# Kernel tuning notes

Hardware: AMD Instinct MI355X
Metric: run time of the kernel (lower is better)

The kernel has to match this reference:

```python
import jax, jax.numpy as jnp
import numpy as np

N = 65536      # total nodes (ground + sub)
NG = 32768     # ground nodes (subnodes are NG..N)
H = 64         # n_hidden
FIN = 32       # n_node_features
L = 2          # num_convolution_blocks
B = 64         # graphs in batch
MAXDEG = 10    # MFConv max_degree -> 11 buckets
EG = 1048576   # ground-graph edges
ES = 1048576   # subgraph edges
EX = 524288    # cross (ground<->sub) edges


def setup_inputs() -> dict:
    key = jax.random.key(0)
    ks = jax.random.split(key, 32)
    NS = N - NG
    x = jax.random.normal(ks[0], (N, FIN), jnp.float32)
    # ground graph: src/dst in [0, NG)
    edge_index = jax.random.randint(ks[1], (2, EG), 0, NG).astype(jnp.int64)
    # subgraph: src/dst in [NG, N)
    subgraph_edge_index = (NG + jax.random.randint(ks[2], (2, ES), 0, NS)).astype(jnp.int64)
    # ground -> sub
    ns_src = jax.random.randint(ks[3], (EX,), 0, NG)
    ns_dst = NG + jax.random.randint(ks[4], (EX,), 0, NS)
    node_subnode_index = jnp.stack([ns_src, ns_dst]).astype(jnp.int64)
    # sub -> ground
    sn_src = NG + jax.random.randint(ks[5], (EX,), 0, NS)
    sn_dst = jax.random.randint(ks[6], (EX,), 0, NG)
    subnode_node_index = jnp.stack([sn_src, sn_dst]).astype(jnp.int64)
    ground_node = jnp.arange(N) < NG
    subgraph_batch_index = jax.random.randint(ks[7], (N,), 0, B).astype(jnp.int64)
    batch_idx = jax.random.randint(ks[8], (N,), 0, B).astype(jnp.int64)
    s = 0.05
    p = {}
    p['embed_W'] = jax.random.normal(ks[9], (FIN, H), jnp.float32) * s
    p['embed_b'] = jnp.zeros((H,), jnp.float32)
    names = ['ground', 'g2s', 'sub', 's2g']
    for i, nm in enumerate(names):
        p[nm + '_Wl'] = jax.random.normal(ks[10 + 3 * i], (L, MAXDEG + 1, H, H), jnp.float32) * s
        p[nm + '_bl'] = jnp.zeros((L, MAXDEG + 1, H), jnp.float32)
        p[nm + '_Wr'] = jax.random.normal(ks[11 + 3 * i], (L, MAXDEG + 1, H, H), jnp.float32) * s
    p['W1'] = jax.random.normal(ks[24], (H, H), jnp.float32) * s
    p['b1'] = jnp.zeros((H,), jnp.float32)
    p['W2'] = jax.random.normal(ks[25], (H, 1), jnp.float32) * s
    p['b2'] = jnp.zeros((1,), jnp.float32)
    return dict(x=x, edge_index=edge_index, subgraph_edge_index=subgraph_edge_index,
                node_subnode_index=node_subnode_index, subnode_node_index=subnode_node_index,
                ground_node=ground_node, subgraph_batch_index=subgraph_batch_index,
                batch_idx=batch_idx, **p)


def _mfconv(h, src, dst, Wl, bl, Wr):
    # PyG MFConv: out_i = Lin_l[deg_i](sum_{j->i} h_j) + Lin_r[deg_i](h_i), deg clamped to MAXDEG
    n = h.shape[0]
    deg = jnp.clip(jax.ops.segment_sum(jnp.ones(src.shape[0], jnp.int32), dst, num_segments=n), 0, MAXDEG)
    agg = jax.ops.segment_sum(h[src], dst, num_segments=n)  # [n, H] sum aggregation
    out = jnp.zeros((n, Wl.shape[-1]), h.dtype)
    for d in range(MAXDEG + 1):
        m = (deg == d)[:, None]
        out = out + jnp.where(m, agg @ Wl[d] + bl[d] + h @ Wr[d], jnp.zeros((), h.dtype))
    return out


def _masked_conv(h, ei, Wl, bl, Wr):
    # nodes that never receive a message keep their old features (catch_lone_sender)
    src, dst = ei[0], ei[1]
    recv = jnp.zeros((h.shape[0],), bool).at[dst].set(True)
    return jnp.where(recv[:, None], _mfconv(h, src, dst, Wl, bl, Wr), h)


def reference(x, edge_index, subgraph_edge_index, node_subnode_index, subnode_node_index,
              ground_node, subgraph_batch_index, batch_idx,
              embed_W, embed_b,
              ground_Wl, ground_bl, ground_Wr,
              g2s_Wl, g2s_bl, g2s_Wr,
              sub_Wl, sub_bl, sub_Wr,
              s2g_Wl, s2g_bl, s2g_Wr,
              W1, b1, W2, b2):
    h = x @ embed_W + embed_b
    for l in range(L):
        if l > 0:
            h = jax.nn.relu(h)
        h = _masked_conv(h, edge_index, ground_Wl[l], ground_bl[l], ground_Wr[l])
        h = _masked_conv(h, node_subnode_index, g2s_Wl[l], g2s_bl[l], g2s_Wr[l])
        h = _masked_conv(h, subgraph_edge_index, sub_Wl[l], sub_bl[l], sub_Wr[l])
        h = _masked_conv(h, subnode_node_index, s2g_Wl[l], s2g_bl[l], s2g_Wr[l])
    # global_add_pool over ground nodes only
    pooled = jax.ops.segment_sum(jnp.where(ground_node[:, None], h, jnp.zeros((), h.dtype)),
                                 batch_idx, num_segments=B)  # [B, H]
    z = jax.nn.relu(pooled @ W1 + b1)
    return z @ W2 + b2  # [B, 1]
```

## Files before the change

kernel.cpp:

```cpp
#include <hip/hip_runtime.h>

#define N_NODES 65536
#define NGROUND 32768
#define NHALF 32768
#define H 64
#define FIN 32
#define NB 64
#define MAXDEG 10
#define RSTRIDE 32769
#define EG 1048576
#define ES 1048576
#define EX 524288
#define TE (EG + EX + ES + EX)
#define BIN2 512
#define NPB 64
#define CHUNK 8192
#define TC 384
#define CNT_LEN 196608
#define NSCANB 192
#define BCAP 6144
#define NEB 2048
#define NFB 32

typedef __attribute__((ext_vector_type(8))) short short8;
typedef __attribute__((ext_vector_type(4))) float f32x4;
typedef __attribute__((ext_vector_type(2))) unsigned int u32x2;
typedef __attribute__((ext_vector_type(4))) unsigned int u32x4;
typedef unsigned short u16;
typedef unsigned int u32;

__device__ __forceinline__ u16 f2bf(float x) {
    unsigned int u = __float_as_uint(x);
    unsigned int r = u + 0x7FFFu + ((u >> 16) & 1u);
    return (u16)(r >> 16);
}
__device__ __forceinline__ float bf2f(u16 b) {
    return __uint_as_float(((unsigned int)b) << 16);
}
__device__ __forceinline__ u32 relu2(u32 w) {
    u32 lo = w & 0xFFFFu;
    if (lo & 0x8000u) lo = 0;
    u32 hi = w >> 16;
    if (hi & 0x8000u) hi = 0;
    return lo | (hi << 16);
}

__device__ __forceinline__ void chunk_resolve(int b, int& set, int& cin,
                                              int& nc, int& base, int& dbase, int& sbase) {
    if (b < 128)      { set = 0; cin = b;       nc = 128; base = 0;      dbase = 0;       sbase = 0; }
    else if (b < 192) { set = 1; cin = b - 128; nc = 64;  base = 65536;  dbase = NGROUND; sbase = 0; }
    else if (b < 320) { set = 2; cin = b - 192; nc = 128; base = 98304;  dbase = NGROUND; sbase = NGROUND; }
    else              { set = 3; cin = b - 320; nc = 64;  base = 163840; dbase = 0;       sbase = NGROUND; }
}

__global__ __launch_bounds__(256) void embed_prep_count_kernel(
    const float* __restrict__ x, const float* __restrict__ W,
    const float* __restrict__ b, u16* __restrict__ hgHi, u16* __restrict__ hsHi,
    const float* W0l, const float* W0r, const float* W1l, const float* W1r,
    const float* W2l, const float* W2r, const float* W3l, const float* W3r,
    short8* __restrict__ fragbuf,
    const int* __restrict__ d0, const int* __restrict__ d1,
    const int* __restrict__ d2, const int* __restrict__ d3,
    int* __restrict__ cnt) {
    int tid = threadIdx.x;
    if (blockIdx.x >= NEB + NFB) {
        __shared__ int hist[BIN2];
        int set, cin, nc, base, dbase, sbase;
        chunk_resolve(blockIdx.x - NEB - NFB, set, cin, nc, base, dbase, sbase);
        const int* dp = set == 0 ? d0 : set == 1 ? d1 : set == 2 ? d2 : d3;
        for (int i = tid; i < BIN2; i += 256) hist[i] = 0;
        __syncthreads();
        int e0 = cin * CHUNK;
        for (int i = tid; i < CHUNK; i += 256) {
            int d = __builtin_nontemporal_load(&dp[e0 + i]) - dbase;
            atomicAdd(&hist[d >> 6], 1);
        }
        __syncthreads();
        for (int i = tid; i < BIN2; i += 256)
            cnt[base + i * nc + cin] = hist[i];
        return;
    }
    if (blockIdx.x >= NEB) {
        int tid2 = (blockIdx.x - NEB) * 256 + tid;
        int lane = tid2 & 63;
        int f8 = (tid2 >> 6) & 7;
        int mat = (tid2 >> 9) & 1;
        int layer = (tid2 >> 10) & 1;
        int set = (tid2 >> 11) & 3;
        int s = f8 >> 2, t = f8 & 3;
        const float* Wb;
        if (set == 0) Wb = mat ? W0r : W0l;
        else if (set == 1) Wb = mat ? W1r : W1l;
        else if (set == 2) Wb = mat ? W2r : W2l;
        else Wb = mat ? W3r : W3l;
        Wb += ((size_t)layer * (MAXDEG + 1) + MAXDEG) * H * H;
        int k0 = s * 32 + (lane >> 4) * 8;
        int n = t * 16 + (lane & 15);
        short8 hi, lo;
#pragma unroll
        for (int j = 0; j < 8; j++) {
            float w = Wb[(size_t)(k0 + j) * H + n];
            u16 hb = f2bf(w);
            u16 lb = f2bf(w - bf2f(hb));
            hi[j] = (short)hb;
            lo[j] = (short)lb;
        }
        size_t basehi = ((size_t)(((set * 2 + layer) * 2 + mat) * 2 + 0) * 8 + f8) * 64 + lane;
        size_t baselo = ((size_t)(((set * 2 + layer) * 2 + mat) * 2 + 1) * 8 + f8) * 64 + lane;
        fragbuf[basehi] = hi;
        fragbuf[baselo] = lo;
        return;
    }
    int f = tid & 63;
    int wy = tid >> 6;
    __shared__ float sW[FIN * H];
    for (int i = tid; i < FIN * H; i += 256) sW[i] = W[i];
    __syncthreads();
    float bf_ = b[f];
#pragma unroll
    for (int it = 0; it < 8; it++) {
        int node = blockIdx.x * 32 + it * 4 + wy;
        const float* xr = x + (size_t)node * FIN;
        float acc = bf_;
#pragma unroll
        for (int k = 0; k < FIN; k++) acc += xr[k] * sW[k * H + f];
        if (node < NGROUND)
            hgHi[(size_t)node * H + f] = f2bf(acc);
        else
            hsHi[(size_t)(node - NGROUND) * H + f] = f2bf(acc);
    }
}

__global__ __launch_bounds__(256) void scanA_kernel(
    int* __restrict__ cnt, int* __restrict__ bsum) {
    __shared__ int lds[256];
    int t = threadIdx.x;
    int base = blockIdx.x * 1024 + t * 4;
    int v0 = cnt[base], v1 = cnt[base + 1], v2 = cnt[base + 2], v3 = cnt[base + 3];
    int s = v0 + v1 + v2 + v3;
    lds[t] = s;
    __syncthreads();
    for (int d = 1; d < 256; d <<= 1) {
        int x = 0;
        if (t >= d) x = lds[t - d];
        __syncthreads();
        lds[t] += x;
        __syncthreads();
    }
    int pref = lds[t] - s;
    cnt[base] = pref;
    cnt[base + 1] = pref + v0;
    cnt[base + 2] = pref + v0 + v1;
    cnt[base + 3] = pref + v0 + v1 + v2;
    if (t == 255) bsum[blockIdx.x] = pref + s;
}

__global__ __launch_bounds__(256) void scanB_kernel(int* __restrict__ bsum) {
    __shared__ int lds[256];
    int t = threadIdx.x;
    int v = (t < NSCANB) ? bsum[t] : 0;
    lds[t] = v;
    __syncthreads();
    for (int d = 1; d < 256; d <<= 1) {
        int x = 0;
        if (t >= d) x = lds[t - d];
        __syncthreads();
        lds[t] += x;
        __syncthreads();
    }
    if (t < NSCANB) bsum[t] = lds[t] - v;
}

__global__ __launch_bounds__(256) void partition_kernel(
    const int* __restrict__ s0, const int* __restrict__ s1,
    const int* __restrict__ s2, const int* __restrict__ s3,
    const int* __restrict__ d0, const int* __restrict__ d1,
    const int* __restrict__ d2, const int* __restrict__ d3,
    const int* __restrict__ cnt, const int* __restrict__ bsum,
    u32* __restrict__ csru) {
    __shared__ u32 buf[CHUNK];
    __shared__ int hist[BIN2];
    __shared__ int lofs[BIN2];
    __shared__ int gbase[BIN2];
    __shared__ int sc[256];
    int set, cin, nc, base, dbase, sbase;
    chunk_resolve(blockIdx.x, set, cin, nc, base, dbase, sbase);
    const int* dp = set == 0 ? d0 : set == 1 ? d1 : set == 2 ? d2 : d3;
    const int* sp = set == 0 ? s0 : set == 1 ? s1 : set == 2 ? s2 : s3;
    int t = threadIdx.x;
    for (int i = t; i < BIN2; i += 256) hist[i] = 0;
    __syncthreads();
    u32 pk[32];
    int e0 = cin * CHUNK;
#pragma unroll
    for (int j = 0; j < 32; j++) {
        int idx = e0 + t + j * 256;
        int d = __builtin_nontemporal_load(&dp[idx]) - dbase;
        int s = __builtin_nontemporal_load(&sp[idx]) - sbase;
        pk[j] = ((u32)d << 15) | (u32)s;
        atomicAdd(&hist[d >> 6], 1);
    }
    __syncthreads();
    int h0 = hist[2 * t], h1 = hist[2 * t + 1];
    int hs = h0 + h1;
    sc[t] = hs;
    __syncthreads();
    for (int d2 = 1; d2 < 256; d2 <<= 1) {
        int v = 0;
        if (t >= d2) v = sc[t - d2];
        __syncthreads();
        sc[t] += v;
        __syncthreads();
    }
    int pref = sc[t] - hs;
    lofs[2 * t] = pref;
    lofs[2 * t + 1] = pref + h0;
    hist[2 * t] = pref;
    hist[2 * t + 1] = pref + h0;
    for (int i = t; i < BIN2; i += 256) {
        int idx = base + i * nc + cin;
        gbase[i] = cnt[idx] + bsum[idx >> 10];
    }
    __syncthreads();
#pragma unroll
    for (int j = 0; j < 32; j++) {
        int bin = pk[j] >> 21;
        int pos = atomicAdd(&hist[bin], 1);
        buf[pos] = pk[j];
    }
    __syncthreads();
    for (int i = t; i < CHUNK; i += 256) {
        u32 pkt = buf[i];
        int d = pkt >> 15;
        int bin = d >> 6;
        int gpos = gbase[bin] + (i - lofs[bin]);
        csru[gpos] = pkt & 0x1FFFFFu;
    }
}

__global__ __launch_bounds__(256) void finalize_kernel(
    u32* __restrict__ csru, const int* __restrict__ cnt,
    const int* __restrict__ bsum, int* __restrict__ rowstart4) {
    __shared__ u32 buf[BCAP];
    __shared__ int deg[NPB], off[NPB];
    int b = blockIdx.x;
    int set = b >> 9, bin = b & 511;
    int nc = (set == 0 || set == 2) ? 128 : 64;
    int base = set == 0 ? 0 : set == 1 ? 65536 : set == 2 ? 98304 : 163840;
    int flat = base + bin * nc;
    int binstart = cnt[flat] + bsum[flat >> 10];
    int binend = (b == 2047) ? TE : (cnt[flat + nc] + bsum[(flat + nc) >> 10]);
    int n = binend - binstart;
    for (int i = threadIdx.x; i < n; i += 256) buf[i] = csru[binstart + i];
    if (threadIdx.x < NPB) deg[threadIdx.x] = 0;
    __syncthreads();
    for (int i = threadIdx.x; i < n; i += 256) atomicAdd(&deg[buf[i] >> 15], 1);
    __syncthreads();
    if (threadIdx.x == 0) {
        int r = 0;
        for (int j = 0; j < NPB; j++) { off[j] = r; r += deg[j]; }
    }
    __syncthreads();
    int coffset = set == 0 ? 0 : set == 1 ? EG : set == 2 ? EG + EX : EG + EX + ES;
    if (threadIdx.x < NPB)
        rowstart4[set * RSTRIDE + bin * NPB + threadIdx.x] =
            binstart - coffset + off[threadIdx.x];
    if (bin == 0 && threadIdx.x == 0)
        rowstart4[set * RSTRIDE + NHALF] = (set == 0 || set == 2) ? EG : EX;
    if (threadIdx.x < NPB) deg[threadIdx.x] = off[threadIdx.x];
    __syncthreads();
    for (int i = threadIdx.x; i < n; i += 256) {
        u32 pkt = buf[i];
        int dl = pkt >> 15;
        int pos = atomicAdd(&deg[dl], 1);
        csru[binstart + pos] = pkt & 0x7FFFu;
    }
}

__global__ __launch_bounds__(256) void conv_fused_kernel(
    const u16* __restrict__ srcHi, const u16* __restrict__ selfHi,
    u16* __restrict__ outHi, const int* __restrict__ csr,
    const int* __restrict__ rowstart, const short8* __restrict__ fragbase,
    const float* __restrict__ Wlp, const float* __restrict__ Wrp,
    const float* __restrict__ blp, int do_relu, u32* __restrict__ relu_buf) {
    if (blockIdx.x >= 2048) {
        int base = ((blockIdx.x - 2048) * 256 + threadIdx.x) * 2;
        u32x4* p = (u32x4*)relu_buf;
        u32x4 a = p[base], b = p[base + 1];
        a.x = relu2(a.x); a.y = relu2(a.y); a.z = relu2(a.z); a.w = relu2(a.w);
        b.x = relu2(b.x); b.y = relu2(b.y); b.z = relu2(b.z); b.w = relu2(b.w);
        p[base] = a;
        p[base + 1] = b;
        return;
    }
    __shared__ u16 sB[4][64][16];
    __shared__ float sAgg[16][68];
    int tid = threadIdx.x;
    int w = tid >> 6, lane = tid & 63;
    int node0 = blockIdx.x * 16;
    int q = lane >> 4, mrow = lane & 15;

    int R0 = rowstart[node0];
    int R16 = rowstart[node0 + 16];
    int rlo = rowstart[node0 + mrow];
    int rhi = rowstart[node0 + mrow + 1];
    u32 rspan = (u32)(rhi - rlo);
    R16 = min(max(R16, R0), R0 + 8192);

    f32x4 aggv = (f32x4){0.f, 0.f, 0.f, 0.f};

    int p_ = lane & 7;
    int e0 = w * 16 + (lane >> 3);
    int e1 = e0 + 8;
    u32 lds_rd = (u32)(uintptr_t)(&sB[w][0][0]) + (u32)lane * 8u;

    for (int ce = R0; ce < R16; ce += 64) {
        int s0 = csr[min(ce + e0, R16 - 1)];
        int s1 = csr[min(ce + e1, R16 - 1)];
        u32x4 va = *((const u32x4*)(srcHi + (size_t)s0 * H) + p_);
        u32x4 vb = *((const u32x4*)(srcHi + (size_t)s1 * H) + p_);
        __syncthreads();
        *(u32x4*)&sB[p_ >> 1][e0][(p_ & 1) * 8] = va;
        *(u32x4*)&sB[p_ >> 1][e1][(p_ & 1) * 8] = vb;
        __syncthreads();
        u32x2 r0, r1, r2, r3;
        asm volatile(
            "ds_read_b64_tr_b16 %0, %4 offset:0\n\t"
            "ds_read_b64_tr_b16 %1, %4 offset:512\n\t"
            "ds_read_b64_tr_b16 %2, %4 offset:1024\n\t"
            "ds_read_b64_tr_b16 %3, %4 offset:1536\n\t"
            "s_waitcnt lgkmcnt(0)"
            : "=&v"(r0), "=&v"(r1), "=&v"(r2), "=&v"(r3)
            : "v"(lds_rd)
            : "memory");
        __builtin_amdgcn_sched_barrier(0);
#pragma unroll
        for (int half = 0; half < 2; half++) {
            int ebase = ce + half * 32 + q * 4;
            short8 Af;
#pragma unroll
            for (int j = 0; j < 8; j++) {
                int E = ebase + ((j < 4) ? j : (12 + j));
                u32 off = (u32)E - (u32)rlo;
                Af[j] = (off < rspan) ? (short)0x3F80 : (short)0;
            }
            union { short8 s; u32 u[4]; } bb;
            if (half == 0) {
                bb.u[0] = r0[0]; bb.u[1] = r0[1];
                bb.u[2] = r1[0]; bb.u[3] = r1[1];
            } else {
                bb.u[0] = r2[0]; bb.u[1] = r2[1];
                bb.u[2] = r3[0]; bb.u[3] = r3[1];
            }
            aggv = __builtin_amdgcn_mfma_f32_16x16x32_bf16(Af, bb.s, aggv, 0, 0, 0);
        }
    }
#pragma unroll
    for (int r = 0; r < 4; r++) sAgg[q * 4 + r][w * 16 + mrow] = aggv[r];
    __syncthreads();

    int myrow = node0 + mrow;
    int mydeg = rhi - rlo;
    unsigned long long ball = __ballot(min(mydeg, MAXDEG) != MAXDEG);
    unsigned exc = (unsigned)(ball & 0xFFFFull);
    int t = w;

    f32x4 accv = (f32x4){0.f, 0.f, 0.f, 0.f};
    const short8* fb = fragbase + lane;
#pragma unroll
    for (int s = 0; s < 2; s++) {
        float av[8];
        *(float4*)&av[0] = *(const float4*)&sAgg[mrow][s * 32 + q * 8];
        *(float4*)&av[4] = *(const float4*)&sAgg[mrow][s * 32 + q * 8 + 4];
        short8 Ahi;
#pragma unroll
        for (int j = 0; j < 8; j++) Ahi[j] = (short)f2bf(av[j]);
        short8 Hhi = *(const short8*)(selfHi + (size_t)myrow * H + s * 32 + q * 8);
        short8 BLhi = fb[(size_t)((0 * 8) + s * 4 + t) * 64];
        short8 BLlo = fb[(size_t)((1 * 8) + s * 4 + t) * 64];
        short8 BRhi = fb[(size_t)((2 * 8) + s * 4 + t) * 64];
        short8 BRlo = fb[(size_t)((3 * 8) + s * 4 + t) * 64];
        accv = __builtin_amdgcn_mfma_f32_16x16x32_bf16(Ahi, BLhi, accv, 0, 0, 0);
        accv = __builtin_amdgcn_mfma_f32_16x16x32_bf16(Ahi, BLlo, accv, 0, 0, 0);
        accv = __builtin_amdgcn_mfma_f32_16x16x32_bf16(Hhi, BRhi, accv, 0, 0, 0);
        accv = __builtin_amdgcn_mfma_f32_16x16x32_bf16(Hhi, BRlo, accv, 0, 0, 0);
    }

    {
        int n = t * 16 + mrow;
        float bv = blp[MAXDEG * H + n];
#pragma unroll
        for (int r = 0; r < 4; r++) {
            int mm = q * 4 + r;
            if (!((exc >> mm) & 1)) {
                float val = accv[r] + bv;
                if (do_relu) val = fmaxf(val, 0.f);
                outHi[(size_t)(node0 + mm) * H + n] = f2bf(val);
            }
        }
    }

    if (exc & (0xFu << (w * 4))) {
        for (int i = 0; i < 4; i++) {
            int nr = w * 4 + i;
            if (!((exc >> nr) & 1)) continue;
            int node = node0 + nr;
            int st = rowstart[node], en = rowstart[node + 1];
            int dg = en - st;
            if (dg == 0) {
                float v = bf2f(selfHi[(size_t)node * H + lane]);
                if (do_relu) v = fmaxf(v, 0.f);
                outHi[(size_t)node * H + lane] = f2bf(v);
            } else {
                int d = min(dg, MAXDEG);
                const float* wl = Wlp + (size_t)d * H * H;
                const float* wr = Wrp + (size_t)d * H * H;
                float sval = bf2f(selfHi[(size_t)node * H + lane]);
                float o = blp[d * H + lane];
#pragma unroll 4
                for (int k = 0; k < H; k++) {
                    o += sAgg[nr][k] * wl[k * H + lane];
                    o += __shfl(sval, k, 64) * wr[k * H + lane];
                }
                if (do_relu) o = fmaxf(o, 0.f);
                outHi[(size_t)node * H + lane] = f2bf(o);
            }
        }
    }
}

__global__ __launch_bounds__(256) void pool_kernel(
    const u16* __restrict__ hgHi, const int* __restrict__ batch_idx,
    float* __restrict__ pooled) {
    __shared__ float lp[NB * H];
    int tid = threadIdx.x;
    for (int i = tid; i < NB * H; i += 256) lp[i] = 0.f;
    __syncthreads();
    int f = tid & 63;
    int wave = tid >> 6;
    int start = blockIdx.x * 64;
    for (int n = wave; n < 64; n += 4) {
        int node = start + n;
        int bi = batch_idx[node];
        atomicAdd(&lp[bi * H + f], bf2f(hgHi[(size_t)node * H + f]));
    }
    __syncthreads();
    for (int i = tid; i < NB * H; i += 256) {
        float v = lp[i];
        if (v != 0.f) atomicAdd(&pooled[i], v);
    }
}

__global__ __launch_bounds__(64) void mlp_kernel(
    const float* __restrict__ pooled, const float* __restrict__ W1,
    const float* __restrict__ b1, const float* __restrict__ W2,
    const float* __restrict__ b2, float* __restrict__ out) {
    int b = blockIdx.x;
    int j = threadIdx.x;
    const float* pr = pooled + b * H;
    float acc = b1[j];
#pragma unroll
    for (int k = 0; k < H; k++) acc += pr[k] * W1[k * H + j];
    acc = fmaxf(acc, 0.f);
    float v = acc * W2[j];
#pragma unroll
    for (int off = 32; off > 0; off >>= 1) v += __shfl_down(v, off, 64);
    if (j == 0) out[b] = v + b2[0];
}

extern "C" void kernel_launch(void* const* d_in, const int* in_sizes, int n_in,
                              void* d_out, int out_size, void* d_ws, size_t ws_size,
                              hipStream_t stream) {
    const float* x = (const float*)d_in[0];
    const int* ei_ground = (const int*)d_in[1];
    const int* ei_sub = (const int*)d_in[2];
    const int* ei_g2s = (const int*)d_in[3];
    const int* ei_s2g = (const int*)d_in[4];
    const int* batch_idx = (const int*)d_in[7];
    const float* embed_W = (const float*)d_in[8];
    const float* embed_b = (const float*)d_in[9];
    const float* Wl[4] = {(const float*)d_in[10], (const float*)d_in[13],
                          (const float*)d_in[16], (const float*)d_in[19]};
    const float* bl[4] = {(const float*)d_in[11], (const float*)d_in[14],
                          (const float*)d_in[17], (const float*)d_in[20]};
    const float* Wr[4] = {(const float*)d_in[12], (const float*)d_in[15],
                          (const float*)d_in[18], (const float*)d_in[21]};
    const float* W1 = (const float*)d_in[22];
    const float* b1 = (const float*)d_in[23];
    const float* W2 = (const float*)d_in[24];
    const float* b2 = (const float*)d_in[25];

    const int* s_[4] = {ei_ground, ei_g2s, ei_sub, ei_s2g};
    const int* dsr[4] = {ei_ground + EG, ei_g2s + EX, ei_sub + ES, ei_s2g + EX};
    const size_t coff[4] = {0, (size_t)EG, (size_t)EG + EX, (size_t)EG + EX + ES};

    const size_t HB = (size_t)NHALF * H * sizeof(u16);
    char* p = (char*)d_ws;
    u16* hgHi[2] = {(u16*)p, (u16*)(p + HB)};            p += 2 * HB;
    u16* hsHi[2] = {(u16*)p, (u16*)(p + HB)};            p += 2 * HB;
    u32* csru = (u32*)p;           p += (size_t)TE * sizeof(u32);
    int* cnt = (int*)p;            p += (size_t)CNT_LEN * sizeof(int);
    int* bsum = (int*)p;           p += (size_t)NSCANB * sizeof(int);
    int* rowstart4 = (int*)p;      p += (size_t)4 * RSTRIDE * sizeof(int);
    p += 16 - ((size_t)p & 15);
    short8* fragbuf = (short8*)p;  p += (size_t)8192 * sizeof(short8);
    float* pooled = (float*)p;

    embed_prep_count_kernel<<<NEB + NFB + TC, 256, 0, stream>>>(
        x, embed_W, embed_b, hgHi[0], hsHi[0],
        Wl[0], Wr[0], Wl[1], Wr[1], Wl[2], Wr[2], Wl[3], Wr[3], fragbuf,
        dsr[0], dsr[1], dsr[2], dsr[3], cnt);

    scanA_kernel<<<NSCANB, 256, 0, stream>>>(cnt, bsum);
    scanB_kernel<<<1, 256, 0, stream>>>(bsum);
    partition_kernel<<<TC, 256, 0, stream>>>(
        s_[0], s_[1], s_[2], s_[3], dsr[0], dsr[1], dsr[2], dsr[3], cnt, bsum, csru);
    finalize_kernel<<<2048, 256, 0, stream>>>(csru, cnt, bsum, rowstart4);
    const int* csr = (const int*)csru;

    int cg = 0, cs = 0;
    for (int l = 0; l < 2; l++) {
        for (int c = 0; c < 4; c++) {
            const u16 *srcHi, *selfHi;
            u16 *outHi;
            if (c == 0)      { srcHi = hgHi[cg]; selfHi = hgHi[cg]; outHi = hgHi[1 - cg]; }
            else if (c == 1) { srcHi = hgHi[cg]; selfHi = hsHi[cs]; outHi = hsHi[1 - cs]; }
            else if (c == 2) { srcHi = hsHi[cs]; selfHi = hsHi[cs]; outHi = hsHi[1 - cs]; }
            else             { srcHi = hsHi[cs]; selfHi = hgHi[cg]; outHi = hgHi[1 - cg]; }
            int do_relu = (l == 0 && c == 3) ? 1 : 0;
            int relu_blocks = (l == 1 && c == 0) ? 512 : 0;
            u32* relu_buf = (l == 1 && c == 0) ? (u32*)hsHi[cs] : (u32*)nullptr;
            conv_fused_kernel<<<2048 + relu_blocks, 256, 0, stream>>>(
                srcHi, selfHi, outHi,
                csr + coff[c], rowstart4 + (size_t)c * RSTRIDE,
                fragbuf + (size_t)(c * 2 + l) * 2048,
                Wl[c] + (size_t)l * (MAXDEG + 1) * H * H,
                Wr[c] + (size_t)l * (MAXDEG + 1) * H * H,
                bl[c] + (size_t)l * (MAXDEG + 1) * H, do_relu, relu_buf);
            if (c == 0 || c == 3) cg ^= 1; else cs ^= 1;
        }
    }

    hipMemsetAsync(pooled, 0, (size_t)NB * H * sizeof(float), stream);
    pool_kernel<<<NGROUND / 64, 256, 0, stream>>>(hgHi[cg], batch_idx, pooled);
    mlp_kernel<<<NB, 64, 0, stream>>>(pooled, W1, b1, W2, b2, (float*)d_out);
}
```

Before: 377.1 us.

## Process 128 edges per gather iteration and alias aggregation LDS buffer

The fused conv kernel's neighbour-gather loop now processes 128 edges per iteration instead of 64. Each thread issues four independent row loads and eight transposed LDS reads, feeding four MFMAs per barrier pair. The sB and sAgg shared arrays are aliased into one buffer, with an extra barrier before sAgg is written, and launch bounds request 8 blocks per CU. The aim is more memory-level parallelism and fewer barriers per edge, at the cost of more wasted padded work for small rows and higher register pressure.

```diff
diff --git a/kernel.cpp b/kernel.cpp
--- a/kernel.cpp
+++ b/kernel.cpp
@@ -277,7 +277,7 @@
     }
 }
 
-__global__ __launch_bounds__(256) void conv_fused_kernel(
+__global__ __launch_bounds__(256, 8) void conv_fused_kernel(
     const u16* __restrict__ srcHi, const u16* __restrict__ selfHi,
     u16* __restrict__ outHi, const int* __restrict__ csr,
     const int* __restrict__ rowstart, const short8* __restrict__ fragbase,
@@ -293,8 +293,9 @@
         p[base + 1] = b;
         return;
     }
-    __shared__ u16 sB[4][64][16];
-    __shared__ float sAgg[16][68];
+    __shared__ __align__(16) char smem[4 * 128 * 16 * 2];
+    u16 (*sB)[128][16] = (u16 (*)[128][16])smem;
+    float (*sAgg)[68] = (float (*)[68])smem;
     int tid = threadIdx.x;
     int w = tid >> 6, lane = tid & 63;
     int node0 = blockIdx.x * 16;
@@ -310,32 +311,42 @@
     f32x4 aggv = (f32x4){0.f, 0.f, 0.f, 0.f};
 
     int p_ = lane & 7;
-    int e0 = w * 16 + (lane >> 3);
-    int e1 = e0 + 8;
+    int eb = w * 32 + (lane >> 3);
     u32 lds_rd = (u32)(uintptr_t)(&sB[w][0][0]) + (u32)lane * 8u;
 
-    for (int ce = R0; ce < R16; ce += 64) {
-        int s0 = csr[min(ce + e0, R16 - 1)];
-        int s1 = csr[min(ce + e1, R16 - 1)];
-        u32x4 va = *((const u32x4*)(srcHi + (size_t)s0 * H) + p_);
-        u32x4 vb = *((const u32x4*)(srcHi + (size_t)s1 * H) + p_);
-        __syncthreads();
-        *(u32x4*)&sB[p_ >> 1][e0][(p_ & 1) * 8] = va;
-        *(u32x4*)&sB[p_ >> 1][e1][(p_ & 1) * 8] = vb;
-        __syncthreads();
-        u32x2 r0, r1, r2, r3;
+    for (int ce = R0; ce < R16; ce += 128) {
+        int s0 = csr[min(ce + eb,      R16 - 1)];
+        int s1 = csr[min(ce + eb + 8,  R16 - 1)];
+        int s2 = csr[min(ce + eb + 16, R16 - 1)];
+        int s3 = csr[min(ce + eb + 24, R16 - 1)];
+        u32x4 v0 = *((const u32x4*)(srcHi + (size_t)s0 * H) + p_);
+        u32x4 v1 = *((const u32x4*)(srcHi + (size_t)s1 * H) + p_);
+        u32x4 v2 = *((const u32x4*)(srcHi + (size_t)s2 * H) + p_);
+        u32x4 v3 = *((const u32x4*)(srcHi + (size_t)s3 * H) + p_);
+        __syncthreads();
+        *(u32x4*)&sB[p_ >> 1][eb][(p_ & 1) * 8] = v0;
+        *(u32x4*)&sB[p_ >> 1][eb + 8][(p_ & 1) * 8] = v1;
+        *(u32x4*)&sB[p_ >> 1][eb + 16][(p_ & 1) * 8] = v2;
+        *(u32x4*)&sB[p_ >> 1][eb + 24][(p_ & 1) * 8] = v3;
+        __syncthreads();
+        u32x2 r0, r1, r2, r3, r4, r5, r6, r7;
         asm volatile(
-            "ds_read_b64_tr_b16 %0, %4 offset:0\n\t"
-            "ds_read_b64_tr_b16 %1, %4 offset:512\n\t"
-            "ds_read_b64_tr_b16 %2, %4 offset:1024\n\t"
-            "ds_read_b64_tr_b16 %3, %4 offset:1536\n\t"
+            "ds_read_b64_tr_b16 %0, %8 offset:0\n\t"
+            "ds_read_b64_tr_b16 %1, %8 offset:512\n\t"
+            "ds_read_b64_tr_b16 %2, %8 offset:1024\n\t"
+            "ds_read_b64_tr_b16 %3, %8 offset:1536\n\t"
+            "ds_read_b64_tr_b16 %4, %8 offset:2048\n\t"
+            "ds_read_b64_tr_b16 %5, %8 offset:2560\n\t"
+            "ds_read_b64_tr_b16 %6, %8 offset:3072\n\t"
+            "ds_read_b64_tr_b16 %7, %8 offset:3584\n\t"
             "s_waitcnt lgkmcnt(0)"
-            : "=&v"(r0), "=&v"(r1), "=&v"(r2), "=&v"(r3)
+            : "=&v"(r0), "=&v"(r1), "=&v"(r2), "=&v"(r3),
+              "=&v"(r4), "=&v"(r5), "=&v"(r6), "=&v"(r7)
             : "v"(lds_rd)
             : "memory");
         __builtin_amdgcn_sched_barrier(0);
 #pragma unroll
-        for (int half = 0; half < 2; half++) {
+        for (int half = 0; half < 4; half++) {
             int ebase = ce + half * 32 + q * 4;
             short8 Af;
 #pragma unroll
@@ -345,16 +356,14 @@
                 Af[j] = (off < rspan) ? (short)0x3F80 : (short)0;
             }
             union { short8 s; u32 u[4]; } bb;
-            if (half == 0) {
-                bb.u[0] = r0[0]; bb.u[1] = r0[1];
-                bb.u[2] = r1[0]; bb.u[3] = r1[1];
-            } else {
-                bb.u[0] = r2[0]; bb.u[1] = r2[1];
-                bb.u[2] = r3[0]; bb.u[3] = r3[1];
-            }
+            u32x2 ra = (half == 0) ? r0 : (half == 1) ? r2 : (half == 2) ? r4 : r6;
+            u32x2 rb = (half == 0) ? r1 : (half == 1) ? r3 : (half == 2) ? r5 : r7;
+            bb.u[0] = ra[0]; bb.u[1] = ra[1];
+            bb.u[2] = rb[0]; bb.u[3] = rb[1];
             aggv = __builtin_amdgcn_mfma_f32_16x16x32_bf16(Af, bb.s, aggv, 0, 0, 0);
         }
     }
+    __syncthreads();
 #pragma unroll
     for (int r = 0; r < 4; r++) sAgg[q * 4 + r][w * 16 + mrow] = aggv[r];
     __syncthreads();
```

Result: no change. 379.5 us (+0.6%).
